# Kernel optimization log

Hardware: AMD Instinct MI355X
Metric: run time of the kernel (lower is better)

## Reference

```python
import jax, jax.numpy as jnp
import numpy as np

NC = 32           # tessellation cells on [0,1]
N_POINTS = 2097152
EPS = 1e-10


def cpa_basis(nc):
    """Orthonormal (SVD) null-space basis of the CPA continuity constraints.
    Each cell c has velocity v(x) = a_c x + b_c; continuity at internal knots
    x_k = k/nc gives (nc-1) constraints on the 2*nc params -> basis (2nc, nc+1)."""
    L = np.zeros((nc - 1, 2 * nc))
    for k in range(1, nc):
        xk = k / nc
        L[k - 1, 2 * (k - 1)] = xk
        L[k - 1, 2 * (k - 1) + 1] = 1.0
        L[k - 1, 2 * k] = -xk
        L[k - 1, 2 * k + 1] = -1.0
    _, _, Vt = np.linalg.svd(L, full_matrices=True)
    return Vt[nc - 1:].T  # (2nc, nc+1)


B_NP = cpa_basis(NC)


def setup_inputs():
    key = jax.random.key(0)
    k1, k2 = jax.random.split(key)
    x = jax.random.uniform(k1, (N_POINTS,), dtype=jnp.float32)
    theta = 0.5 * jax.random.normal(k2, (1, NC + 1), dtype=jnp.float32)
    return {"x": x, "theta": theta}


def _transform(x, theta):
    """Closed-form CPAB integration: phi(x) = solution at t=1 of dphi/dt = v(phi),
    v piecewise affine. Within a cell the ODE has a closed form; a trajectory is
    monotone so it crosses each of the NC cells at most once -> scan of NC steps.
    Also accumulates log|dphi/dx| = integral of a(phi(s)) ds in closed form."""
    nc = NC
    h = 1.0 / nc
    A = (jnp.asarray(B_NP, x.dtype) @ theta[0]).reshape(nc, 2)  # per-cell (a, b)
    c0 = jnp.clip(jnp.floor(x * nc).astype(jnp.int32), 0, nc - 1)
    t0 = jnp.ones_like(x)      # remaining integration time
    lj0 = jnp.zeros_like(x)    # accumulated log-Jacobian

    def step(state, _):
        xs, t, c, lj = state
        a = A[c, 0]
        b = A[c, 1]
        v = a * xs + b
        # boundary in direction of motion (extreme cells extend to +/- inf)
        left = jnp.where(c == 0, -jnp.inf, c * h)
        right = jnp.where(c == nc - 1, jnp.inf, (c + 1) * h)
        xc = jnp.where(v > 0, right, left)
        finite = jnp.isfinite(xc)
        xcs = jnp.where(finite, xc, xs)
        big = jnp.abs(a) > EPS
        a_s = jnp.where(big, a, 1.0)
        # time to hit boundary: exp(a t) = v(xc)/v(x) (a != 0), (xc-x)/b (a == 0)
        vc = a * xcs + b
        r = vc / jnp.where(v == 0, 1.0, v)
        th_a = jnp.log(jnp.maximum(r, EPS)) / a_s
        th_b = (xcs - xs) / jnp.where(jnp.abs(b) > EPS, b, 1.0)
        t_hit = jnp.where(big, jnp.where(r > EPS, th_a, jnp.inf), th_b)
        valid = finite & (v != 0) & (t_hit > 0)
        t_hit = jnp.where(valid, t_hit, jnp.inf)
        cross = t_hit < t
        dt = jnp.where(cross, jnp.where(jnp.isfinite(t_hit), t_hit, 0.0), t)
        # closed-form in-cell flow psi(x, dt)
        psi = jnp.where(big, jnp.exp(a * dt) * (xs + b / a_s) - b / a_s, xs + b * dt)
        x_new = jnp.where(cross, xcs, psi)
        lj_new = lj + a * dt
        t_new = jnp.where(cross, t - dt, 0.0)
        c_new = jnp.clip(c + jnp.where(cross, jnp.where(v > 0, 1, -1), 0), 0, nc - 1)
        return (x_new, t_new, c_new, lj_new), None

    (z, _, _, lj), _ = jax.lax.scan(step, (x, t0, c0, lj0), None, length=nc)
    return z, lj


def reference(x, theta):
    z, log_dz_dx = _transform(x, theta)
    return (z, log_dz_dx)
```

## Files before the change

### kernel.cpp

```cpp
#include <hip/hip_runtime.h>
#include <math.h>

#define NCC  32
#define EPSF 1e-10f
#define TPB  512

struct MTab { float mt[33][64]; };

constexpr double csqrt_(double x) {
    double y = x > 1.0 ? x : 1.0;
    for (int i = 0; i < 80; ++i) y = 0.5 * (y + x / y);
    return y;
}

constexpr MTab make_mtab() {
    double Lm[31][64] = {};
    for (int k = 1; k < 32; ++k) {
        double xk = (double)k / 32.0;
        Lm[k - 1][2 * (k - 1)]     = xk;
        Lm[k - 1][2 * (k - 1) + 1] = 1.0;
        Lm[k - 1][2 * k]           = -xk;
        Lm[k - 1][2 * k + 1]       = -1.0;
    }
    double tau[31] = {};
    for (int i = 0; i < 31; ++i) {
        int E = 2 * i + 3; if (E > 63) E = 63;
        double xn2 = 0.0;
        for (int p = i + 1; p <= E; ++p) xn2 += Lm[i][p] * Lm[i][p];
        const double alpha = Lm[i][i];
        double tu = 0.0, sc = 0.0;
        if (xn2 != 0.0) {
            const double nrm  = csqrt_(alpha * alpha + xn2);
            const double beta = (alpha >= 0.0) ? -nrm : nrm;
            tu = (beta - alpha) / beta;
            sc = 1.0 / (alpha - beta);
        }
        for (int p = i + 1; p <= E; ++p) Lm[i][p] *= sc;
        Lm[i][i] = 1.0;
        tau[i] = tu;
        for (int j = i + 1; j < 31; ++j) {
            double s = 0.0;
            for (int p = i; p <= E; ++p) s += Lm[i][p] * Lm[j][p];
            s *= tu;
            for (int p = i; p <= E; ++p) Lm[j][p] -= s * Lm[i][p];
        }
    }
    MTab o{};
    for (int col = 0; col < 33; ++col) {
        double u[64] = {};
        u[31 + col] = 1.0;
        for (int i = 30; i >= 0; --i) {
            int E = 2 * i + 3; if (E > 63) E = 63;
            double s = 0.0;
            for (int p = i; p <= E; ++p) s += Lm[i][p] * u[p];
            s *= tau[i];
            for (int p = i; p <= E; ++p) u[p] -= s * Lm[i][p];
        }
        for (int p = 0; p < 64; ++p) o.mt[col][p] = (float)u[p];
    }
    return o;
}

__constant__ const MTab dM = make_mtab();

__global__ __launch_bounds__(TPB) void cpab_flow(const float* __restrict__ x_in,
                                                 const float* __restrict__ theta,
                                                 float* __restrict__ out, int n) {
    __shared__ float sA[64];
    __shared__ float aS[NCC], bS[NCC], boaS[NCC], vLS[NCC], vRS[NCC], laS[NCC];
    __shared__ float thf[2][NCC], ljf[2][NCC];
    __shared__ float Sa[2 * NCC][33];
    __shared__ float La[2 * NCC][33];

    const int   tid = threadIdx.x;
    const float INF = __builtin_inff();

    if (tid < 64) {
        float acc = 0.0f;
#pragma unroll
        for (int j = 0; j < 33; ++j) acc = fmaf(dM.mt[j][tid], theta[j], acc);
        sA[tid] = acc;
    }
    __syncthreads();
    if (tid < NCC) {
        const float a   = sA[2 * tid];
        const float b   = sA[2 * tid + 1];
        const bool  big = fabsf(a) > EPSF;
        aS[tid]   = a;
        bS[tid]   = b;
        boaS[tid] = b / (big ? a : 1.0f);
        laS[tid]  = (float)(0.6931471805599453094 / (double)(big ? a : 1.0f));
        vLS[tid]  = __fadd_rn(__fmul_rn(a, __fmul_rn((float)tid,       0.03125f)), b);
        vRS[tid]  = __fadd_rn(__fmul_rn(a, __fmul_rn((float)(tid + 1), 0.03125f)), b);
    }
    __syncthreads();
    if (tid < 2 * NCC) {
        const int   c     = tid & 31;
        const int   dd    = tid >> 5;
        const float a     = aS[c];
        const float b     = bS[c];
        const float entry = __fmul_rn((float)(c + (dd ? 0 : 1)), 0.03125f);
        const float v     = dd ? vLS[c] : vRS[c];
        const bool  dirA  = v > 0.0f;
        const bool  fin   = dirA ? (c < NCC - 1) : (c > 0);
        const float xb    = __fmul_rn((float)(c + (dirA ? 1 : 0)), 0.03125f);
        const float xcs   = fin ? xb : entry;
        const float vc    = fin ? (dirA ? vRS[c] : vLS[c]) : v;
        const bool  v0    = (v == 0.0f);
        const float r     = vc / (v0 ? 1.0f : v);
        const bool  big   = fabsf(a) > EPSF;
        const float a_s   = big ? a : 1.0f;
        const float th_a  = logf(fmaxf(r, EPSF)) / a_s;
        const float bb    = (fabsf(b) > EPSF) ? b : 1.0f;
        const float th_b  = __fsub_rn(xcs, entry) / bb;
        float t_hit = big ? ((r > EPSF) ? th_a : INF) : th_b;
        const bool valid = fin && !v0 && (t_hit > 0.0f);
        t_hit = valid ? t_hit : INF;
        thf[dd][c] = t_hit;
        ljf[dd][c] = __fmul_rn(a, t_hit);
    }
    __syncthreads();
    if (tid < 2 * NCC) {
        const int d  = tid >> 5;
        const int c1 = tid & 31;
        const int dh = d ? 1 : -1;
        float S = 0.0f, LJ = 0.0f;
        Sa[tid][0] = 0.0f;
        La[tid][0] = 0.0f;
#pragma unroll
        for (int k = 1; k <= 32; ++k) {
            const int cell = c1 + (k - 1) * dh;
            float th = 4.0f, lp = 0.0f;
            if (cell >= 0 && cell < NCC) {
                th = thf[d][cell];
                lp = ljf[d][cell];
                if (!(th <= 2.0f)) { th = 4.0f; lp = 0.0f; }
            }
            S  = __fadd_rn(S, th);
            LJ = __fadd_rn(LJ, lp);
            Sa[tid][k] = S;
            La[tid][k] = LJ;
        }
    }
    __syncthreads();

    const int ti   = blockIdx.x * blockDim.x + tid;
    const int base = ti << 2;
    if (base >= n) return;
    const bool full = (base + 3 < n);

    float4 xv;
    if (full) {
        xv = *reinterpret_cast<const float4*>(x_in + base);
    } else {
        xv.x = x_in[base];
        xv.y = (base + 1 < n) ? x_in[base + 1] : 0.0f;
        xv.z = (base + 2 < n) ? x_in[base + 2] : 0.0f;
        xv.w = 0.0f;
    }
    float4 zo, jo;

#pragma unroll
    for (int q = 0; q < 4; ++q) {
        const float x0 = (q == 0) ? xv.x : (q == 1) ? xv.y : (q == 2) ? xv.z : xv.w;
        int c0 = (int)floorf(__fmul_rn(x0, 32.0f));
        c0 = min(max(c0, 0), NCC - 1);

        const float a    = aS[c0];
        const float b    = bS[c0];
        const float v    = __fadd_rn(__fmul_rn(a, x0), b);
        const bool  dirA = v > 0.0f;
        const bool  fin  = dirA ? (c0 < NCC - 1) : (c0 > 0);
        const float xb   = __fmul_rn((float)(c0 + (dirA ? 1 : 0)), 0.03125f);
        const float xcs  = fin ? xb : x0;
        const float vc   = fin ? (dirA ? vRS[c0] : vLS[c0]) : v;
        const bool  v0   = (v == 0.0f);
        const float r    = vc / (v0 ? 1.0f : v);
        const bool  big  = fabsf(a) > EPSF;
        const float th_a = __builtin_amdgcn_logf(fmaxf(r, EPSF)) * laS[c0];
        float th_b = 0.0f;
        if (__any(!big)) {
            const float bb = (fabsf(b) > EPSF) ? b : 1.0f;
            th_b = __fsub_rn(xcs, x0) / bb;
        }
        float th = big ? ((r > EPSF) ? th_a : INF) : th_b;
        const bool valid = fin && !v0 && (th > 0.0f);
        th = valid ? th : INF;

        const bool  cross0 = th < 1.0f;
        const float t0     = __fsub_rn(1.0f, th);
        const float lj0    = __fmul_rn(a, th);
        const int   dh     = dirA ? 1 : -1;
        const int   c1     = c0 + dh;
        const int   c1c    = min(max(c1, 0), NCC - 1);
        const int   row    = (dirA ? NCC : 0) + c1c;

        int m = 0;
#pragma unroll
        for (int s = 32; s >= 1; s >>= 1) {
            const int   cand  = m + s;
            const int   candc = min(cand, 32);
            const float u     = Sa[row][candc];
            m = ((cand <= 32) && (t0 > u)) ? cand : m;
        }
        const float Sm = Sa[row][m];
        const float Lm = La[row][m];

        const float t  = cross0 ? __fsub_rn(t0, Sm) : 1.0f;
        const float lj = cross0 ? __fadd_rn(lj0, Lm) : 0.0f;
        int cf = cross0 ? (c1 + m * dh) : c0;
        cf = min(max(cf, 0), NCC - 1);
        const float xs = cross0 ? __fmul_rn((float)(cf + (dirA ? 0 : 1)), 0.03125f)
                                : x0;

        const float af   = aS[cf];
        const float bf   = bS[cf];
        const bool  bigf = fabsf(af) > EPSF;
        const float boa  = boaS[cf];
        const float ad   = __fmul_rn(af, t);
        const float ea   = __builtin_amdgcn_exp2f(__fmul_rn(ad, 1.44269504088896340736f));
        const float psi  = bigf ? __fsub_rn(__fmul_rn(ea, __fadd_rn(xs, boa)), boa)
                                : __fadd_rn(xs, __fmul_rn(bf, t));
        const float ljo  = __fadd_rn(lj, ad);
        if (q == 0) { zo.x = psi; jo.x = ljo; }
        if (q == 1) { zo.y = psi; jo.y = ljo; }
        if (q == 2) { zo.z = psi; jo.z = ljo; }
        if (q == 3) { zo.w = psi; jo.w = ljo; }
    }

    if (full) {
        *reinterpret_cast<float4*>(out + base)     = zo;
        *reinterpret_cast<float4*>(out + n + base) = jo;
    } else {
        out[base] = zo.x;             out[n + base] = jo.x;
        if (base + 1 < n) { out[base + 1] = zo.y; out[n + base + 1] = jo.y; }
        if (base + 2 < n) { out[base + 2] = zo.z; out[n + base + 2] = jo.z; }
    }
}

extern "C" void kernel_launch(void* const* d_in, const int* in_sizes, int n_in,
                              void* d_out, int out_size, void* d_ws, size_t ws_size,
                              hipStream_t stream) {
    (void)d_ws; (void)ws_size; (void)n_in; (void)out_size;
    const float* x     = (const float*)d_in[0];
    const float* theta = (const float*)d_in[1];
    float*       out   = (float*)d_out;
    const int    n     = in_sizes[0];

    const int threads4 = (n + 3) >> 2;
    const int blocks   = (threads4 + TPB - 1) / TPB;
    cpab_flow<<<blocks, TPB, 0, stream>>>(x, theta, out, n);
}
```

Before: 18.63 us.

## Pack cell table into float4, vectorize prefix search, hoist input load

```diff
diff --git a/kernel.cpp b/kernel.cpp
--- a/kernel.cpp
+++ b/kernel.cpp
@@ -4,6 +4,7 @@
 #define NCC  32
 #define EPSF 1e-10f
 #define TPB  512
+#define SROW 36
 
 struct MTab { float mt[33][64]; };
 
@@ -66,14 +67,21 @@
 __global__ __launch_bounds__(TPB) void cpab_flow(const float* __restrict__ x_in,
                                                  const float* __restrict__ theta,
                                                  float* __restrict__ out, int n) {
-    __shared__ float sA[64];
-    __shared__ float aS[NCC], bS[NCC], boaS[NCC], vLS[NCC], vRS[NCC], laS[NCC];
-    __shared__ float thf[2][NCC], ljf[2][NCC];
-    __shared__ float Sa[2 * NCC][33];
-    __shared__ float La[2 * NCC][33];
+    __shared__ float  sA[64];
+    __shared__ float4 cellT[NCC];
+    __shared__ float  laS[NCC], boaS[NCC];
+    __shared__ float  thf[2][NCC], ljf[2][NCC];
+    __shared__ __align__(16) float SaR[64 * SROW];
+    __shared__ __align__(16) float LaR[64 * SROW];
 
     const int   tid = threadIdx.x;
     const float INF = __builtin_inff();
+
+    const int ti   = blockIdx.x * TPB + tid;
+    const int base = ti << 2;
+    float4 xv = make_float4(0.0f, 0.0f, 0.0f, 0.0f);
+    const bool inb = (base + 3 < n);
+    if (inb) xv = *reinterpret_cast<const float4*>(x_in + base);
 
     if (tid < 64) {
         float acc = 0.0f;
@@ -86,33 +94,33 @@
         const float a   = sA[2 * tid];
         const float b   = sA[2 * tid + 1];
         const bool  big = fabsf(a) > EPSF;
-        aS[tid]   = a;
-        bS[tid]   = b;
-        boaS[tid] = b / (big ? a : 1.0f);
-        laS[tid]  = (float)(0.6931471805599453094 / (double)(big ? a : 1.0f));
-        vLS[tid]  = __fadd_rn(__fmul_rn(a, __fmul_rn((float)tid,       0.03125f)), b);
-        vRS[tid]  = __fadd_rn(__fmul_rn(a, __fmul_rn((float)(tid + 1), 0.03125f)), b);
+        const float vL  = __fadd_rn(__fmul_rn(a, __fmul_rn((float)tid,       0.03125f)), b);
+        const float vR  = __fadd_rn(__fmul_rn(a, __fmul_rn((float)(tid + 1), 0.03125f)), b);
+        cellT[tid] = make_float4(a, b, vL, vR);
+        boaS[tid]  = b / (big ? a : 1.0f);
+        laS[tid]   = (float)(0.6931471805599453094 / (double)(big ? a : 1.0f));
     }
     __syncthreads();
     if (tid < 2 * NCC) {
-        const int   c     = tid & 31;
-        const int   dd    = tid >> 5;
-        const float a     = aS[c];
-        const float b     = bS[c];
-        const float entry = __fmul_rn((float)(c + (dd ? 0 : 1)), 0.03125f);
-        const float v     = dd ? vLS[c] : vRS[c];
-        const bool  dirA  = v > 0.0f;
-        const bool  fin   = dirA ? (c < NCC - 1) : (c > 0);
-        const float xb    = __fmul_rn((float)(c + (dirA ? 1 : 0)), 0.03125f);
-        const float xcs   = fin ? xb : entry;
-        const float vc    = fin ? (dirA ? vRS[c] : vLS[c]) : v;
-        const bool  v0    = (v == 0.0f);
-        const float r     = vc / (v0 ? 1.0f : v);
-        const bool  big   = fabsf(a) > EPSF;
-        const float a_s   = big ? a : 1.0f;
-        const float th_a  = logf(fmaxf(r, EPSF)) / a_s;
-        const float bb    = (fabsf(b) > EPSF) ? b : 1.0f;
-        const float th_b  = __fsub_rn(xcs, entry) / bb;
+        const int    c     = tid & 31;
+        const int    dd    = tid >> 5;
+        const float4 ct    = cellT[c];
+        const float  a     = ct.x;
+        const float  b     = ct.y;
+        const float  entry = __fmul_rn((float)(c + (dd ? 0 : 1)), 0.03125f);
+        const float  v     = dd ? ct.z : ct.w;
+        const bool   dirA  = v > 0.0f;
+        const bool   fin   = dirA ? (c < NCC - 1) : (c > 0);
+        const float  xb    = __fmul_rn((float)(c + (dirA ? 1 : 0)), 0.03125f);
+        const float  xcs   = fin ? xb : entry;
+        const float  vc    = fin ? (dirA ? ct.w : ct.z) : v;
+        const bool   v0    = (v == 0.0f);
+        const float  r     = vc / (v0 ? 1.0f : v);
+        const bool   big   = fabsf(a) > EPSF;
+        const float  a_s   = big ? a : 1.0f;
+        const float  th_a  = logf(fmaxf(r, EPSF)) / a_s;
+        const float  bb    = (fabsf(b) > EPSF) ? b : 1.0f;
+        const float  th_b  = __fsub_rn(xcs, entry) / bb;
         float t_hit = big ? ((r > EPSF) ? th_a : INF) : th_b;
         const bool valid = fin && !v0 && (t_hit > 0.0f);
         t_hit = valid ? t_hit : INF;
@@ -121,43 +129,35 @@
     }
     __syncthreads();
     if (tid < 2 * NCC) {
-        const int d  = tid >> 5;
+        const int dd = tid >> 5;
         const int c1 = tid & 31;
-        const int dh = d ? 1 : -1;
-        float S = 0.0f, LJ = 0.0f;
-        Sa[tid][0] = 0.0f;
-        La[tid][0] = 0.0f;
-#pragma unroll
-        for (int k = 1; k <= 32; ++k) {
-            const int cell = c1 + (k - 1) * dh;
+        const int dh = dd ? 1 : -1;
+        float thv[32], ljv[32];
+#pragma unroll
+        for (int k = 0; k < 32; ++k) {
+            const int cell = c1 + k * dh;
             float th = 4.0f, lp = 0.0f;
             if (cell >= 0 && cell < NCC) {
-                th = thf[d][cell];
-                lp = ljf[d][cell];
+                th = thf[dd][cell];
+                lp = ljf[dd][cell];
                 if (!(th <= 2.0f)) { th = 4.0f; lp = 0.0f; }
             }
-            S  = __fadd_rn(S, th);
-            LJ = __fadd_rn(LJ, lp);
-            Sa[tid][k] = S;
-            La[tid][k] = LJ;
-        }
-    }
-    __syncthreads();
-
-    const int ti   = blockIdx.x * blockDim.x + tid;
-    const int base = ti << 2;
+            thv[k] = th; ljv[k] = lp;
+        }
+        float S = 0.0f, LJ = 0.0f;
+        float* Sr = SaR + tid * SROW;
+        float* Lr = LaR + tid * SROW;
+#pragma unroll
+        for (int k = 0; k < 32; ++k) {
+            S  = __fadd_rn(S, thv[k]);
+            LJ = __fadd_rn(LJ, ljv[k]);
+            Sr[k] = S;
+            Lr[k] = LJ;
+        }
+    }
+    __syncthreads();
+
     if (base >= n) return;
-    const bool full = (base + 3 < n);
-
-    float4 xv;
-    if (full) {
-        xv = *reinterpret_cast<const float4*>(x_in + base);
-    } else {
-        xv.x = x_in[base];
-        xv.y = (base + 1 < n) ? x_in[base + 1] : 0.0f;
-        xv.z = (base + 2 < n) ? x_in[base + 2] : 0.0f;
-        xv.w = 0.0f;
-    }
     float4 zo, jo;
 
 #pragma unroll
@@ -166,18 +166,19 @@
         int c0 = (int)floorf(__fmul_rn(x0, 32.0f));
         c0 = min(max(c0, 0), NCC - 1);
 
-        const float a    = aS[c0];
-        const float b    = bS[c0];
-        const float v    = __fadd_rn(__fmul_rn(a, x0), b);
-        const bool  dirA = v > 0.0f;
-        const bool  fin  = dirA ? (c0 < NCC - 1) : (c0 > 0);
-        const float xb   = __fmul_rn((float)(c0 + (dirA ? 1 : 0)), 0.03125f);
-        const float xcs  = fin ? xb : x0;
-        const float vc   = fin ? (dirA ? vRS[c0] : vLS[c0]) : v;
-        const bool  v0   = (v == 0.0f);
-        const float r    = vc / (v0 ? 1.0f : v);
-        const bool  big  = fabsf(a) > EPSF;
-        const float th_a = __builtin_amdgcn_logf(fmaxf(r, EPSF)) * laS[c0];
+        const float4 ct   = cellT[c0];
+        const float  a    = ct.x;
+        const float  b    = ct.y;
+        const float  v    = __fadd_rn(__fmul_rn(a, x0), b);
+        const bool   dirA = v > 0.0f;
+        const bool   fin  = dirA ? (c0 < NCC - 1) : (c0 > 0);
+        const float  xb   = __fmul_rn((float)(c0 + (dirA ? 1 : 0)), 0.03125f);
+        const float  xcs  = fin ? xb : x0;
+        const float  vc   = fin ? (dirA ? ct.w : ct.z) : v;
+        const bool   v0   = (v == 0.0f);
+        const float  r    = vc / (v0 ? 1.0f : v);
+        const bool   big  = fabsf(a) > EPSF;
+        const float  th_a = __builtin_amdgcn_logf(fmaxf(r, EPSF)) * laS[c0];
         float th_b = 0.0f;
         if (__any(!big)) {
             const float bb = (fabsf(b) > EPSF) ? b : 1.0f;
@@ -195,16 +196,19 @@
         const int   c1c    = min(max(c1, 0), NCC - 1);
         const int   row    = (dirA ? NCC : 0) + c1c;
 
+        const float* Sr = SaR + row * SROW;
         int m = 0;
 #pragma unroll
-        for (int s = 32; s >= 1; s >>= 1) {
-            const int   cand  = m + s;
-            const int   candc = min(cand, 32);
-            const float u     = Sa[row][candc];
-            m = ((cand <= 32) && (t0 > u)) ? cand : m;
-        }
-        const float Sm = Sa[row][m];
-        const float Lm = La[row][m];
+        for (int kk = 0; kk < 8; ++kk) {
+            const float4 s4 = *reinterpret_cast<const float4*>(Sr + kk * 4);
+            m += (t0 > s4.x) ? 1 : 0;
+            m += (t0 > s4.y) ? 1 : 0;
+            m += (t0 > s4.z) ? 1 : 0;
+            m += (t0 > s4.w) ? 1 : 0;
+        }
+        const int   mi = (m > 0) ? (m - 1) : 0;
+        const float Sm = (m > 0) ? Sr[mi] : 0.0f;
+        const float Lm = (m > 0) ? LaR[row * SROW + mi] : 0.0f;
 
         const float t  = cross0 ? __fsub_rn(t0, Sm) : 1.0f;
         const float lj = cross0 ? __fadd_rn(lj0, Lm) : 0.0f;
@@ -213,28 +217,23 @@
         const float xs = cross0 ? __fmul_rn((float)(cf + (dirA ? 0 : 1)), 0.03125f)
                                 : x0;
 
-        const float af   = aS[cf];
-        const float bf   = bS[cf];
-        const bool  bigf = fabsf(af) > EPSF;
-        const float boa  = boaS[cf];
-        const float ad   = __fmul_rn(af, t);
-        const float ea   = __builtin_amdgcn_exp2f(__fmul_rn(ad, 1.44269504088896340736f));
-        const float psi  = bigf ? __fsub_rn(__fmul_rn(ea, __fadd_rn(xs, boa)), boa)
-                                : __fadd_rn(xs, __fmul_rn(bf, t));
-        const float ljo  = __fadd_rn(lj, ad);
+        const float4 cf4  = cellT[cf];
+        const bool   bigf = fabsf(cf4.x) > EPSF;
+        const float  boa  = boaS[cf];
+        const float  ad   = __fmul_rn(cf4.x, t);
+        const float  ea   = __builtin_amdgcn_exp2f(__fmul_rn(ad, 1.44269504088896340736f));
+        const float  psi  = bigf ? __fsub_rn(__fmul_rn(ea, __fadd_rn(xs, boa)), boa)
+                                 : __fadd_rn(xs, __fmul_rn(cf4.y, t));
+        const float  ljo  = __fadd_rn(lj, ad);
         if (q == 0) { zo.x = psi; jo.x = ljo; }
         if (q == 1) { zo.y = psi; jo.y = ljo; }
         if (q == 2) { zo.z = psi; jo.z = ljo; }
         if (q == 3) { zo.w = psi; jo.w = ljo; }
     }
 
-    if (full) {
+    if (inb) {
         *reinterpret_cast<float4*>(out + base)     = zo;
         *reinterpret_cast<float4*>(out + n + base) = jo;
-    } else {
-        out[base] = zo.x;             out[n + base] = jo.x;
-        if (base + 1 < n) { out[base + 1] = zo.y; out[n + base + 1] = jo.y; }
-        if (base + 2 < n) { out[base + 2] = zo.z; out[n + base + 2] = jo.z; }
     }
 }
 
```

After: 21.90 us. 17.6% more time.

## Split table setup into separate kernel and replace binary search with lookup table

Applied to the files above, without the earlier changes.

```diff
diff --git a/kernel.cpp b/kernel.cpp
--- a/kernel.cpp
+++ b/kernel.cpp
@@ -4,6 +4,13 @@
 #define NCC  32
 #define EPSF 1e-10f
 #define TPB  512
+
+#define WOFF_CAB 0
+#define WOFF_TA  64
+#define WOFF_AF  192
+#define WOFF_SL  320
+#define WOFF_MT  4544
+#define WTOT     6592
 
 struct MTab { float mt[33][64]; };
 
@@ -63,15 +70,12 @@
 
 __constant__ const MTab dM = make_mtab();
 
-__global__ __launch_bounds__(TPB) void cpab_flow(const float* __restrict__ x_in,
-                                                 const float* __restrict__ theta,
-                                                 float* __restrict__ out, int n) {
-    __shared__ float sA[64];
-    __shared__ float aS[NCC], bS[NCC], boaS[NCC], vLS[NCC], vRS[NCC], laS[NCC];
-    __shared__ float thf[2][NCC], ljf[2][NCC];
-    __shared__ float Sa[2 * NCC][33];
-    __shared__ float La[2 * NCC][33];
-
+__global__ __launch_bounds__(TPB) void cpab_setup(const float* __restrict__ theta,
+                                                  float* __restrict__ W) {
+    __shared__ float  sA[64];
+    __shared__ float  aS[NCC], bS[NCC], vLS[NCC], vRS[NCC], laS[NCC];
+    __shared__ float  thf[2][NCC], ljf[2][NCC];
+    __shared__ float2 SLs[64][33];
     const int   tid = threadIdx.x;
     const float INF = __builtin_inff();
 
@@ -86,12 +90,17 @@
         const float a   = sA[2 * tid];
         const float b   = sA[2 * tid + 1];
         const bool  big = fabsf(a) > EPSF;
-        aS[tid]   = a;
-        bS[tid]   = b;
-        boaS[tid] = b / (big ? a : 1.0f);
-        laS[tid]  = (float)(0.6931471805599453094 / (double)(big ? a : 1.0f));
-        vLS[tid]  = __fadd_rn(__fmul_rn(a, __fmul_rn((float)tid,       0.03125f)), b);
-        vRS[tid]  = __fadd_rn(__fmul_rn(a, __fmul_rn((float)(tid + 1), 0.03125f)), b);
+        const float vL  = __fadd_rn(__fmul_rn(a, __fmul_rn((float)tid,       0.03125f)), b);
+        const float vR  = __fadd_rn(__fmul_rn(a, __fmul_rn((float)(tid + 1), 0.03125f)), b);
+        const float boa = b / (big ? a : 1.0f);
+        aS[tid] = a; bS[tid] = b; vLS[tid] = vL; vRS[tid] = vR;
+        laS[tid] = (float)(0.6931471805599453094 / (double)(big ? a : 1.0f));
+        W[WOFF_CAB + 2 * tid]     = a;
+        W[WOFF_CAB + 2 * tid + 1] = b;
+        W[WOFF_AF + 4 * tid]     = a;
+        W[WOFF_AF + 4 * tid + 1] = boa;
+        W[WOFF_AF + 4 * tid + 2] = b;
+        W[WOFF_AF + 4 * tid + 3] = 0.0f;
     }
     __syncthreads();
     if (tid < 2 * NCC) {
@@ -118,46 +127,83 @@
         t_hit = valid ? t_hit : INF;
         thf[dd][c] = t_hit;
         ljf[dd][c] = __fmul_rn(a, t_hit);
+        const int rowT = dd * 32 + c;
+        W[WOFF_TA + 2 * rowT]     = dd ? vRS[c] : vLS[c];
+        W[WOFF_TA + 2 * rowT + 1] = laS[c];
     }
     __syncthreads();
     if (tid < 2 * NCC) {
-        const int d  = tid >> 5;
-        const int c1 = tid & 31;
-        const int dh = d ? 1 : -1;
+        const int dd = tid >> 5, c1 = tid & 31, dh = dd ? 1 : -1;
         float S = 0.0f, LJ = 0.0f;
-        Sa[tid][0] = 0.0f;
-        La[tid][0] = 0.0f;
+        SLs[tid][0] = make_float2(0.0f, 0.0f);
 #pragma unroll
         for (int k = 1; k <= 32; ++k) {
             const int cell = c1 + (k - 1) * dh;
             float th = 4.0f, lp = 0.0f;
             if (cell >= 0 && cell < NCC) {
-                th = thf[d][cell];
-                lp = ljf[d][cell];
+                th = thf[dd][cell];
+                lp = ljf[dd][cell];
                 if (!(th <= 2.0f)) { th = 4.0f; lp = 0.0f; }
             }
             S  = __fadd_rn(S, th);
             LJ = __fadd_rn(LJ, lp);
-            Sa[tid][k] = S;
-            La[tid][k] = LJ;
-        }
-    }
-    __syncthreads();
-
-    const int ti   = blockIdx.x * blockDim.x + tid;
+            SLs[tid][k] = make_float2(S, LJ);
+        }
+        for (int k = 0; k <= 32; ++k) {
+            W[WOFF_SL + (tid * 33 + k) * 2]     = SLs[tid][k].x;
+            W[WOFF_SL + (tid * 33 + k) * 2 + 1] = SLs[tid][k].y;
+        }
+    }
+    __syncthreads();
+    {
+        const int e0  = tid * 16;
+        const int row = e0 >> 7;
+        unsigned int packs[4] = {0, 0, 0, 0};
+#pragma unroll
+        for (int j = 0; j < 16; ++j) {
+            const int   u  = (e0 + j) & 127;
+            const float tu = __fmul_rn((float)u, 0.0078125f);
+            int lo = 0;
+#pragma unroll
+            for (int s = 32; s >= 1; s >>= 1) {
+                const int cand = lo + s;
+                if (cand <= 32 && SLs[row][cand].x < tu) lo = cand;
+            }
+            packs[j >> 2] |= ((unsigned)lo) << ((j & 3) * 8);
+        }
+        unsigned int* Wm = reinterpret_cast<unsigned int*>(W + WOFF_MT);
+#pragma unroll
+        for (int j = 0; j < 4; ++j) Wm[tid * 4 + j] = packs[j];
+    }
+}
+
+__global__ __launch_bounds__(TPB) void cpab_main(const float* __restrict__ x_in,
+                                                 const float* __restrict__ W,
+                                                 float* __restrict__ out, int n) {
+    __shared__ __align__(16) float LW[WTOT];
+    const int   tid = threadIdx.x;
+    const float INF = __builtin_inff();
+
+    const int ti   = blockIdx.x * TPB + tid;
     const int base = ti << 2;
+    float4 xv = make_float4(0.0f, 0.0f, 0.0f, 0.0f);
+    const bool inb = (base + 3 < n);
+    if (inb) xv = *reinterpret_cast<const float4*>(x_in + base);
+
+    {
+        const float4* Wv = reinterpret_cast<const float4*>(W);
+        float4*       Lv = reinterpret_cast<float4*>(LW);
+        for (int i = tid; i < WTOT / 4; i += TPB) Lv[i] = Wv[i];
+    }
+    __syncthreads();
+
+    const float2* cAB = reinterpret_cast<const float2*>(LW + WOFF_CAB);
+    const float2* tA  = reinterpret_cast<const float2*>(LW + WOFF_TA);
+    const float4* aF  = reinterpret_cast<const float4*>(LW + WOFF_AF);
+    const float2* SL  = reinterpret_cast<const float2*>(LW + WOFF_SL);
+    const unsigned char* mt = reinterpret_cast<const unsigned char*>(LW + WOFF_MT);
+
     if (base >= n) return;
-    const bool full = (base + 3 < n);
-
-    float4 xv;
-    if (full) {
-        xv = *reinterpret_cast<const float4*>(x_in + base);
-    } else {
-        xv.x = x_in[base];
-        xv.y = (base + 1 < n) ? x_in[base + 1] : 0.0f;
-        xv.z = (base + 2 < n) ? x_in[base + 2] : 0.0f;
-        xv.w = 0.0f;
-    }
     float4 zo, jo;
 
 #pragma unroll
@@ -166,21 +212,20 @@
         int c0 = (int)floorf(__fmul_rn(x0, 32.0f));
         c0 = min(max(c0, 0), NCC - 1);
 
-        const float a    = aS[c0];
-        const float b    = bS[c0];
-        const float v    = __fadd_rn(__fmul_rn(a, x0), b);
-        const bool  dirA = v > 0.0f;
-        const bool  fin  = dirA ? (c0 < NCC - 1) : (c0 > 0);
-        const float xb   = __fmul_rn((float)(c0 + (dirA ? 1 : 0)), 0.03125f);
-        const float xcs  = fin ? xb : x0;
-        const float vc   = fin ? (dirA ? vRS[c0] : vLS[c0]) : v;
-        const bool  v0   = (v == 0.0f);
-        const float r    = vc / (v0 ? 1.0f : v);
-        const bool  big  = fabsf(a) > EPSF;
-        const float th_a = __builtin_amdgcn_logf(fmaxf(r, EPSF)) * laS[c0];
+        const float2 ab   = cAB[c0];
+        const float  v    = __fadd_rn(__fmul_rn(ab.x, x0), ab.y);
+        const bool   dirA = v > 0.0f;
+        const bool   fin  = dirA ? (c0 < NCC - 1) : (c0 > 0);
+        const bool   v0   = (v == 0.0f);
+        const bool   big  = fabsf(ab.x) > EPSF;
+        const float2 ta   = tA[(dirA ? 32 : 0) + c0];
+        const float  vc   = fin ? ta.x : v;
+        const float  r    = vc / (v0 ? 1.0f : v);
+        const float  th_a = __builtin_amdgcn_logf(fmaxf(r, EPSF)) * ta.y;
         float th_b = 0.0f;
         if (__any(!big)) {
-            const float bb = (fabsf(b) > EPSF) ? b : 1.0f;
+            const float xcs = fin ? __fmul_rn((float)(c0 + (dirA ? 1 : 0)), 0.03125f) : x0;
+            const float bb  = (fabsf(ab.y) > EPSF) ? ab.y : 1.0f;
             th_b = __fsub_rn(xcs, x0) / bb;
         }
         float th = big ? ((r > EPSF) ? th_a : INF) : th_b;
@@ -188,51 +233,44 @@
         th = valid ? th : INF;
 
         const bool  cross0 = th < 1.0f;
-        const float t0     = __fsub_rn(1.0f, th);
-        const float lj0    = __fmul_rn(a, th);
+        const float t0v    = __fsub_rn(1.0f, th);
+        const float lj0    = __fmul_rn(ab.x, th);
         const int   dh     = dirA ? 1 : -1;
         const int   c1     = c0 + dh;
         const int   c1c    = min(max(c1, 0), NCC - 1);
-        const int   row    = (dirA ? NCC : 0) + c1c;
-
-        int m = 0;
-#pragma unroll
-        for (int s = 32; s >= 1; s >>= 1) {
-            const int   cand  = m + s;
-            const int   candc = min(cand, 32);
-            const float u     = Sa[row][candc];
-            m = ((cand <= 32) && (t0 > u)) ? cand : m;
-        }
-        const float Sm = Sa[row][m];
-        const float Lm = La[row][m];
-
-        const float t  = cross0 ? __fsub_rn(t0, Sm) : 1.0f;
-        const float lj = cross0 ? __fadd_rn(lj0, Lm) : 0.0f;
+        const int   row    = (dirA ? 32 : 0) + c1c;
+
+        int u = (int)__fmul_rn(fmaxf(t0v, 0.0f), 128.0f);
+        u = min(u, 127);
+        int m = (int)mt[(row << 7) + u];
+        while (m < 32 && t0v > SL[row * 33 + m + 1].x) ++m;
+        const float2 slm = SL[row * 33 + m];
+
+        const float tt = cross0 ? __fsub_rn(t0v, slm.x) : 1.0f;
+        const float lj = cross0 ? __fadd_rn(lj0, slm.y) : 0.0f;
         int cf = cross0 ? (c1 + m * dh) : c0;
         cf = min(max(cf, 0), NCC - 1);
         const float xs = cross0 ? __fmul_rn((float)(cf + (dirA ? 0 : 1)), 0.03125f)
                                 : x0;
 
-        const float af   = aS[cf];
-        const float bf   = bS[cf];
-        const bool  bigf = fabsf(af) > EPSF;
-        const float boa  = boaS[cf];
-        const float ad   = __fmul_rn(af, t);
-        const float ea   = __builtin_amdgcn_exp2f(__fmul_rn(ad, 1.44269504088896340736f));
-        const float psi  = bigf ? __fsub_rn(__fmul_rn(ea, __fadd_rn(xs, boa)), boa)
-                                : __fadd_rn(xs, __fmul_rn(bf, t));
-        const float ljo  = __fadd_rn(lj, ad);
+        const float4 af   = aF[cf];
+        const bool   bigf = fabsf(af.x) > EPSF;
+        const float  ad   = __fmul_rn(af.x, tt);
+        const float  ea   = __builtin_amdgcn_exp2f(__fmul_rn(ad, 1.44269504088896340736f));
+        const float  psi  = bigf ? __fsub_rn(__fmul_rn(ea, __fadd_rn(xs, af.y)), af.y)
+                                 : __fadd_rn(xs, __fmul_rn(af.z, tt));
+        const float  ljo  = __fadd_rn(lj, ad);
         if (q == 0) { zo.x = psi; jo.x = ljo; }
         if (q == 1) { zo.y = psi; jo.y = ljo; }
         if (q == 2) { zo.z = psi; jo.z = ljo; }
         if (q == 3) { zo.w = psi; jo.w = ljo; }
     }
 
-    if (full) {
+    if (inb) {
         *reinterpret_cast<float4*>(out + base)     = zo;
         *reinterpret_cast<float4*>(out + n + base) = jo;
     } else {
-        out[base] = zo.x;             out[n + base] = jo.x;
+        if (base < n)     { out[base]     = zo.x; out[n + base]     = jo.x; }
         if (base + 1 < n) { out[base + 1] = zo.y; out[n + base + 1] = jo.y; }
         if (base + 2 < n) { out[base + 2] = zo.z; out[n + base + 2] = jo.z; }
     }
@@ -241,13 +279,15 @@
 extern "C" void kernel_launch(void* const* d_in, const int* in_sizes, int n_in,
                               void* d_out, int out_size, void* d_ws, size_t ws_size,
                               hipStream_t stream) {
-    (void)d_ws; (void)ws_size; (void)n_in; (void)out_size;
+    (void)ws_size; (void)n_in; (void)out_size;
     const float* x     = (const float*)d_in[0];
     const float* theta = (const float*)d_in[1];
     float*       out   = (float*)d_out;
+    float*       W     = (float*)d_ws;
     const int    n     = in_sizes[0];
 
+    cpab_setup<<<1, TPB, 0, stream>>>(theta, W);
     const int threads4 = (n + 3) >> 2;
     const int blocks   = (threads4 + TPB - 1) / TPB;
-    cpab_flow<<<blocks, TPB, 0, stream>>>(x, theta, out, n);
-}
+    cpab_main<<<blocks, TPB, 0, stream>>>(x, W, out, n);
+}
```

Result: slower. 24.99 us (+34.2%).
